# Kernel tuning notes

Measured on AMD Instinct MI355X. Metric: run time of the kernel, lower is better.

The kernel has to match this reference:

```python
import jax, jax.numpy as jnp
import numpy as np

B, S, C = 4, 4096, 1024   # batch, input_size (seq len), channels
H, D, DK = 16, 64, 256    # nhead, head dim, dim_k (Linformer projection)


def setup_inputs() -> dict:
    key = jax.random.key(0)
    ks = jax.random.split(key, 9)
    s_in = 1.0 / np.sqrt(C)
    s_e = 1.0 / np.sqrt(S)
    return {
        'x':   jax.random.normal(ks[0], (B, S, C), jnp.float32),
        # per-head Q/K/V projection weights (Linear(channels, dim, bias=False))
        'Wq':  jax.random.normal(ks[1], (H, D, C), jnp.float32) * s_in,
        'Wk':  jax.random.normal(ks[2], (H, D, C), jnp.float32) * s_in,
        'Wv':  jax.random.normal(ks[3], (H, D, C), jnp.float32) * s_in,
        # shared (layerwise) E/F Linear(input_size, dim_k) with bias
        'E_w': jax.random.normal(ks[4], (DK, S), jnp.float32) * s_e,
        'E_b': jnp.zeros((DK,), jnp.float32),
        'F_w': jax.random.normal(ks[5], (DK, S), jnp.float32) * s_e,
        'F_b': jnp.zeros((DK,), jnp.float32),
        # output projection Linear(dim*nhead, channels)
        'Wo':  jax.random.normal(ks[6], (C, H * D), jnp.float32) * (1.0 / np.sqrt(H * D)),
        'bo':  jnp.zeros((C,), jnp.float32),
    }


def reference(x, Wq, Wk, Wv, E_w, E_b, F_w, F_b, Wo, bo):
    b, s, c = x.shape
    h, d, _ = Wq.shape
    # per-head projections (vectorized over the Python head loop)
    Q = jnp.einsum('bsc,hdc->bhsd', x, Wq)            # [B,H,S,D]
    Kt = jnp.einsum('bsc,hdc->bhds', x, Wk)           # K already transposed: [B,H,D,S]
    Vt = jnp.einsum('bsc,hdc->bhds', x, Wv)           # [B,H,D,S]
    # Linformer low-rank projections along the sequence axis
    Kp = jnp.einsum('bhds,ks->bhdk', Kt, E_w) + E_b   # [B,H,D,DK]
    Vp = jnp.einsum('bhds,ks->bhdk', Vt, F_w) + F_b   # [B,H,D,DK]
    scores = jnp.einsum('bhsd,bhdk->bhsk', Q, Kp) / jnp.sqrt(jnp.asarray(d, x.dtype))
    P = jax.nn.softmax(scores, axis=-1)               # softmax over projected dim_k
    head_out = jnp.einsum('bhsk,bhdk->bhsd', P, Vp)   # [B,H,S,D]
    out = head_out.transpose(0, 2, 1, 3).reshape(b, s, h * d)  # concat heads
    return out @ Wo.T + bo
```

## Files before the change

### kernel.cpp

```cpp
#include <hip/hip_runtime.h>
#include <stdint.h>

typedef __attribute__((ext_vector_type(8))) short bf16x8;
typedef __attribute__((ext_vector_type(4))) float f32x4;
typedef __attribute__((ext_vector_type(16))) float f32x16;

__device__ __forceinline__ unsigned short f2b(float f) {
  union { float f; uint32_t u; } v; v.f = f;
  uint32_t u = v.u;
  return (unsigned short)((u + 0x7FFFu + ((u >> 16) & 1u)) >> 16);
}

__device__ __forceinline__ void gll16(const unsigned short* gsrc, unsigned short* lds_uniform) {
  __builtin_amdgcn_global_load_lds(
      (const __attribute__((address_space(1))) uint32_t*)gsrc,
      (__attribute__((address_space(3))) uint32_t*)lds_uniform,
      16, 0, 0);
}

#define MFMA(a, b, c) __builtin_amdgcn_mfma_f32_16x16x32_bf16((a), (b), (c), 0, 0, 0)
#define MFMA32(a, b, c) __builtin_amdgcn_mfma_f32_32x32x16_bf16((a), (b), (c), 0, 0, 0)

__global__ void cast_x_dual(const float* __restrict__ x,
                            unsigned short* __restrict__ xb,
                            unsigned short* __restrict__ xT) {
  __shared__ unsigned short tile[64][65];
  const int st = blockIdx.x * 64;
  const int ct = blockIdx.y * 64;
  const int b = blockIdx.z;
  const int t = threadIdx.x;
#pragma unroll
  for (int it = 0; it < 4; ++it) {
    int linear = (it * 256 + t) * 4;
    int r = linear >> 6, c = linear & 63;
    float4 v = *(const float4*)(x + ((size_t)(b * 4096 + st + r)) * 1024 + ct + c);
    ushort4 o;
    o.x = f2b(v.x); o.y = f2b(v.y); o.z = f2b(v.z); o.w = f2b(v.w);
    *(ushort4*)(xb + ((size_t)(b * 4096 + st + r)) * 1024 + ct + c) = o;
    tile[r][c] = o.x; tile[r][c + 1] = o.y; tile[r][c + 2] = o.z; tile[r][c + 3] = o.w;
  }
  __syncthreads();
#pragma unroll
  for (int it = 0; it < 4; ++it) {
    int linear = (it * 256 + t) * 4;
    int r = linear >> 6, c = linear & 63;
    ushort4 o;
    o.x = tile[c][r]; o.y = tile[c + 1][r]; o.z = tile[c + 2][r]; o.w = tile[c + 3][r];
    *(ushort4*)(xT + ((size_t)b * 1024 + ct + r) * 4096 + st + c) = o;
  }
}

__global__ void cast6(const float* __restrict__ s0, const float* __restrict__ s1,
                      const float* __restrict__ s2, const float* __restrict__ s3,
                      const float* __restrict__ s4, const float* __restrict__ s5,
                      const float* __restrict__ E_b, const float* __restrict__ F_b,
                      unsigned short* __restrict__ d0, unsigned short* __restrict__ d1,
                      unsigned short* __restrict__ d2, unsigned short* __restrict__ d3,
                      unsigned short* __restrict__ d4, unsigned short* __restrict__ d5,
                      float* __restrict__ EFbias) {
  if (blockIdx.y == 6) {
    if (blockIdx.x == 0) {
      int t = threadIdx.x;
      EFbias[t] = E_b[t];
      EFbias[256 + t] = F_b[t];
    }
    return;
  }
  const float* src; unsigned short* dst; float sc = 1.0f;
  switch (blockIdx.y) {
    case 0: src = s0; dst = d0; sc = 0.18033688011112042f; break;
    case 1: src = s1; dst = d1; break;
    case 2: src = s2; dst = d2; break;
    case 3: src = s3; dst = d3; break;
    case 4: src = s4; dst = d4; break;
    default: src = s5; dst = d5; break;
  }
  int i = (blockIdx.x * 256 + threadIdx.x) * 4;
  float4 v = *(const float4*)(src + i);
  ushort4 o;
  o.x = f2b(v.x * sc); o.y = f2b(v.y * sc); o.z = f2b(v.z * sc); o.w = f2b(v.w * sc);
  *(ushort4*)(dst + i) = o;
}

template <int BIAS, bool OBF16>
__global__ __launch_bounds__(256, 2) void gemm_bt(
    const unsigned short* __restrict__ A, const unsigned short* __restrict__ B,
    void* __restrict__ Cout, const float* __restrict__ bias,
    int M, int N, int K, int lda, int ldb, int ldc,
    long long sA, long long sB, long long sC) {
  __shared__ unsigned short Asm_[2][128 * 32];
  __shared__ unsigned short Bsm_[2][128 * 32];
  const int tid = threadIdx.x;
  const int wave = tid >> 6, lane = tid & 63;
  const int g = lane >> 4, l15 = lane & 15;
  const int bm = blockIdx.x * 128, bn = blockIdx.y * 128;
  const unsigned short* Ab = A + (size_t)blockIdx.z * sA;
  const unsigned short* Bb = B + (size_t)blockIdx.z * sB;
  const int wm = (wave >> 1) * 64, wn = (wave & 1) * 64;

  const int rr0 = wave * 16 + (lane >> 2);
  const int rr1 = rr0 + 64;
  const int sl0 = (lane & 3) ^ ((rr0 >> 1) & 3);
  const int sl1 = (lane & 3) ^ ((rr1 >> 1) & 3);

#define BT_STAGE(T, BUF)                                                          \
  {                                                                               \
    int kt_ = (T) * 32;                                                           \
    gll16(Ab + (size_t)(bm + rr0) * lda + kt_ + sl0 * 8, Asm_[BUF] + wave * 512); \
    gll16(Bb + (size_t)(bn + rr0) * ldb + kt_ + sl0 * 8, Bsm_[BUF] + wave * 512); \
    gll16(Ab + (size_t)(bm + rr1) * lda + kt_ + sl1 * 8, Asm_[BUF] + (wave + 4) * 512); \
    gll16(Bb + (size_t)(bn + rr1) * ldb + kt_ + sl1 * 8, Bsm_[BUF] + (wave + 4) * 512); \
  }

  f32x4 acc[4][4];
#pragma unroll
  for (int i = 0; i < 4; ++i)
#pragma unroll
    for (int j = 0; j < 4; ++j) acc[i][j] = (f32x4){0.f, 0.f, 0.f, 0.f};

  const int nt = K >> 5;
  BT_STAGE(0, 0);
  for (int t = 0; t < nt; ++t) {
    const int cur = t & 1;
    if (t + 1 < nt) {
      BT_STAGE(t + 1, cur ^ 1);
      asm volatile("s_waitcnt vmcnt(4)" ::: "memory");
    } else {
      asm volatile("s_waitcnt vmcnt(0)" ::: "memory");
    }
    __builtin_amdgcn_s_barrier();
    asm volatile("" ::: "memory");

    bf16x8 af[4], bfr[4];
    const char* Ac = (const char*)Asm_[cur];
    const char* Bc = (const char*)Bsm_[cur];
#pragma unroll
    for (int mi = 0; mi < 4; ++mi) {
      int m = wm + mi * 16 + l15;
      af[mi] = *(const bf16x8*)(Ac + m * 64 + ((g ^ ((m >> 1) & 3)) << 4));
    }
#pragma unroll
    for (int ni = 0; ni < 4; ++ni) {
      int n = wn + ni * 16 + l15;
      bfr[ni] = *(const bf16x8*)(Bc + n * 64 + ((g ^ ((n >> 1) & 3)) << 4));
    }
#pragma unroll
    for (int mi = 0; mi < 4; ++mi)
#pragma unroll
      for (int ni = 0; ni < 4; ++ni)
        acc[mi][ni] = MFMA(af[mi], bfr[ni], acc[mi][ni]);

    asm volatile("" ::: "memory");
    __builtin_amdgcn_s_barrier();
  }
#undef BT_STAGE

  if (OBF16) {
    unsigned short* C = (unsigned short*)Cout + (size_t)blockIdx.z * sC;
#pragma unroll
    for (int mi = 0; mi < 4; ++mi)
#pragma unroll
      for (int r = 0; r < 4; ++r) {
        int row = bm + wm + mi * 16 + g * 4 + r;
        float rb = (BIAS == 1) ? bias[row] : 0.f;
#pragma unroll
        for (int ni = 0; ni < 4; ++ni) {
          int col = bn + wn + ni * 16 + l15;
          float v = acc[mi][ni][r] + rb + ((BIAS == 2) ? bias[col] : 0.f);
          C[(size_t)row * ldc + col] = f2b(v);
        }
      }
  } else {
    float* C = (float*)Cout + (size_t)blockIdx.z * sC;
#pragma unroll
    for (int mi = 0; mi < 4; ++mi)
#pragma unroll
      for (int r = 0; r < 4; ++r) {
        int row = bm + wm + mi * 16 + g * 4 + r;
        float rb = (BIAS == 1) ? bias[row] : 0.f;
#pragma unroll
        for (int ni = 0; ni < 4; ++ni) {
          int col = bn + wn + ni * 16 + l15;
          C[(size_t)row * ldc + col] = acc[mi][ni][r] + rb + ((BIAS == 2) ? bias[col] : 0.f);
        }
      }
  }
}

__global__ __launch_bounds__(256, 2) void gemm_xef_splitk(
    const unsigned short* __restrict__ A,
    const unsigned short* __restrict__ B,
    float* __restrict__ Cpart) {
  __shared__ unsigned short Asm_[2][128 * 32];
  __shared__ unsigned short Bsm_[2][128 * 32];
  const int tid = threadIdx.x;
  const int wave = tid >> 6, lane = tid & 63;
  const int g = lane >> 4, l15 = lane & 15;
  const int bm = blockIdx.x * 128, bn = blockIdx.y * 128;
  const int z = blockIdx.z, split = z >> 2, b = z & 3;
  const unsigned short* Ab = A + split * 1024;
  const unsigned short* Bb = B + (size_t)b * 1024 * 4096 + split * 1024;
  const int wm = (wave >> 1) * 64, wn = (wave & 1) * 64;

  const int rr0 = wave * 16 + (lane >> 2);
  const int rr1 = rr0 + 64;
  const int sl0 = (lane & 3) ^ ((rr0 >> 1) & 3);
  const int sl1 = (lane & 3) ^ ((rr1 >> 1) & 3);

#define XEF_STAGE(T, BUF)                                                           \
  {                                                                                 \
    int kt_ = (T) * 32;                                                             \
    gll16(Ab + (size_t)(bm + rr0) * 4096 + kt_ + sl0 * 8, Asm_[BUF] + wave * 512);  \
    gll16(Bb + (size_t)(bn + rr0) * 4096 + kt_ + sl0 * 8, Bsm_[BUF] + wave * 512);  \
    gll16(Ab + (size_t)(bm + rr1) * 4096 + kt_ + sl1 * 8, Asm_[BUF] + (wave + 4) * 512); \
    gll16(Bb + (size_t)(bn + rr1) * 4096 + kt_ + sl1 * 8, Bsm_[BUF] + (wave + 4) * 512); \
  }

  f32x4 acc[4][4];
#pragma unroll
  for (int i = 0; i < 4; ++i)
#pragma unroll
    for (int j = 0; j < 4; ++j) acc[i][j] = (f32x4){0.f, 0.f, 0.f, 0.f};

  const int nt = 32;
  XEF_STAGE(0, 0);
  for (int t = 0; t < nt; ++t) {
    const int cur = t & 1;
    if (t + 1 < nt) {
      XEF_STAGE(t + 1, cur ^ 1);
      asm volatile("s_waitcnt vmcnt(4)" ::: "memory");
    } else {
      asm volatile("s_waitcnt vmcnt(0)" ::: "memory");
    }
    __builtin_amdgcn_s_barrier();
    asm volatile("" ::: "memory");

    bf16x8 af[4], bfr[4];
    const char* Ac = (const char*)Asm_[cur];
    const char* Bc = (const char*)Bsm_[cur];
#pragma unroll
    for (int mi = 0; mi < 4; ++mi) {
      int m = wm + mi * 16 + l15;
      af[mi] = *(const bf16x8*)(Ac + m * 64 + ((g ^ ((m >> 1) & 3)) << 4));
    }
#pragma unroll
    for (int ni = 0; ni < 4; ++ni) {
      int n = wn + ni * 16 + l15;
      bfr[ni] = *(const bf16x8*)(Bc + n * 64 + ((g ^ ((n >> 1) & 3)) << 4));
    }
#pragma unroll
    for (int mi = 0; mi < 4; ++mi)
#pragma unroll
      for (int ni = 0; ni < 4; ++ni)
        acc[mi][ni] = MFMA(af[mi], bfr[ni], acc[mi][ni]);

    asm volatile("" ::: "memory");
    __builtin_amdgcn_s_barrier();
  }
#undef XEF_STAGE

  float* C = Cpart + (size_t)z * (512 * 1024);
#pragma unroll
  for (int mi = 0; mi < 4; ++mi)
#pragma unroll
    for (int r = 0; r < 4; ++r) {
      int row = bm + wm + mi * 16 + g * 4 + r;
#pragma unroll
      for (int ni = 0; ni < 4; ++ni) {
        int col = bn + wn + ni * 16 + l15;
        C[(size_t)row * 1024 + col] = acc[mi][ni][r];
      }
    }
}

__global__ void reduce_xef(const float* __restrict__ P,
                           const float* __restrict__ bias,
                           unsigned short* __restrict__ out) {
  int t = blockIdx.x * 256 + threadIdx.x;
  size_t flat = (size_t)t * 4;
  float4 s = *(const float4*)(P + flat);
#pragma unroll
  for (int sp = 1; sp < 4; ++sp) {
    float4 v = *(const float4*)(P + (size_t)sp * 2097152 + flat);
    s.x += v.x; s.y += v.y; s.z += v.z; s.w += v.w;
  }
  float rb = bias[(flat >> 10) & 511];
  ushort4 o;
  o.x = f2b(s.x + rb); o.y = f2b(s.y + rb);
  o.z = f2b(s.z + rb); o.w = f2b(s.w + rb);
  *(ushort4*)(out + flat) = o;
}

template <int BIAS, bool OBF16, int CMODE>
__global__ __launch_bounds__(256, 4) void gemm_bt64(
    const unsigned short* __restrict__ A, const unsigned short* __restrict__ B,
    void* __restrict__ Cout, const float* __restrict__ bias,
    int M, int N, int K, int lda, int ldb, int ldc,
    long long sA, long long sB, long long sC) {
  __shared__ unsigned short Asm_[2][64 * 32];
  __shared__ unsigned short Bsm_[2][64 * 32];
  const int tid = threadIdx.x;
  const int wave = tid >> 6, lane = tid & 63;
  const int g = lane >> 4, l15 = lane & 15;
  const int bm = blockIdx.x * 64, bn = blockIdx.y * 64;
  const unsigned short* Ab = A + (size_t)blockIdx.z * sA;
  const unsigned short* Bb = B + (size_t)blockIdx.z * sB;
  const int wm = (wave >> 1) * 32, wn = (wave & 1) * 32;

  const int rr = wave * 16 + (lane >> 2);
  const int sl = (lane & 3) ^ ((rr >> 1) & 3);

#define BT64_STAGE(T, BUF)                                                      \
  {                                                                             \
    int kt_ = (T) * 32;                                                         \
    gll16(Ab + (size_t)(bm + rr) * lda + kt_ + sl * 8, Asm_[BUF] + wave * 512); \
    gll16(Bb + (size_t)(bn + rr) * ldb + kt_ + sl * 8, Bsm_[BUF] + wave * 512); \
  }

  f32x4 acc[2][2];
#pragma unroll
  for (int i = 0; i < 2; ++i)
#pragma unroll
    for (int j = 0; j < 2; ++j) acc[i][j] = (f32x4){0.f, 0.f, 0.f, 0.f};

  const int nt = K >> 5;
  BT64_STAGE(0, 0);
  for (int t = 0; t < nt; ++t) {
    const int cur = t & 1;
    if (t + 1 < nt) {
      BT64_STAGE(t + 1, cur ^ 1);
      asm volatile("s_waitcnt vmcnt(2)" ::: "memory");
    } else {
      asm volatile("s_waitcnt vmcnt(0)" ::: "memory");
    }
    __builtin_amdgcn_s_barrier();
    asm volatile("" ::: "memory");

    bf16x8 af[2], bfr[2];
    const char* Ac = (const char*)Asm_[cur];
    const char* Bc = (const char*)Bsm_[cur];
#pragma unroll
    for (int mi = 0; mi < 2; ++mi) {
      int m = wm + mi * 16 + l15;
      af[mi] = *(const bf16x8*)(Ac + m * 64 + ((g ^ ((m >> 1) & 3)) << 4));
    }
#pragma unroll
    for (int ni = 0; ni < 2; ++ni) {
      int n = wn + ni * 16 + l15;
      bfr[ni] = *(const bf16x8*)(Bc + n * 64 + ((g ^ ((n >> 1) & 3)) << 4));
    }
#pragma unroll
    for (int mi = 0; mi < 2; ++mi)
#pragma unroll
      for (int ni = 0; ni < 2; ++ni)
        acc[mi][ni] = MFMA(af[mi], bfr[ni], acc[mi][ni]);

    asm volatile("" ::: "memory");
    __builtin_amdgcn_s_barrier();
  }
#undef BT64_STAGE

#pragma unroll
  for (int mi = 0; mi < 2; ++mi)
#pragma unroll
    for (int r = 0; r < 4; ++r) {
      int row = bm + wm + mi * 16 + g * 4 + r;
      float rb = (BIAS == 1) ? bias[row] : 0.f;
#pragma unroll
      for (int ni = 0; ni < 2; ++ni) {
        int col = bn + wn + ni * 16 + l15;
        float v = acc[mi][ni][r] + rb + ((BIAS == 2) ? bias[col] : 0.f);
        size_t idx;
        if (CMODE == 1) {
          idx = (size_t)(col >> 6) * ((size_t)M * 64) + (size_t)row * 64 + (col & 63);
        } else if (CMODE == 2) {
          int cl = col & 15;
          int cp = (cl & 3) | ((cl & 4) << 1) | ((cl & 8) >> 1);
          idx = (size_t)row * ldc + (col & ~15) + cp;
        } else {
          idx = (size_t)row * ldc + col;
        }
        if (OBF16) ((unsigned short*)Cout + (size_t)blockIdx.z * sC)[idx] = f2b(v);
        else       ((float*)Cout + (size_t)blockIdx.z * sC)[idx] = v;
      }
    }
}

__global__ __launch_bounds__(256, 4) void attn_kernel(
    const unsigned short* __restrict__ q,
    const unsigned short* __restrict__ kp,
    const unsigned short* __restrict__ vp,
    unsigned short* __restrict__ ho) {
  __shared__ unsigned short Ksm[256 * 64];
  __shared__ float Lsm[4 * 32];

  const int tid = threadIdx.x;
  const int wave = tid >> 6, lane = tid & 63;
  const int l31 = lane & 31, hi = lane >> 5;
  const int x = blockIdx.x;
  const int bh = (x & 7) + ((x >> 8) << 3);
  const int qq = (x >> 3) & 31;
  const int b = bh >> 4, h = bh & 15;
  const int s0 = qq * 128;

  const unsigned short* kph = kp + (size_t)bh * (256 * 64);
  const unsigned short* vph = vp + (size_t)bh * (64 * 256);

  {
    const int r = (lane >> 3), sl = (lane & 7) ^ (lane >> 3);
#pragma unroll
    for (int it = 0; it < 8; ++it) {
      int c = it * 4 + wave;
      gll16(kph + (c * 8 + r) * 64 + sl * 8, Ksm + c * 512);
    }
  }

  const int srow = s0 + wave * 32 + l31;
  const unsigned short* qrow = q + (size_t)(b * 4096 + srow) * 1024 + h * 64;
  bf16x8 qf[4];
#pragma unroll
  for (int dc = 0; dc < 4; ++dc)
    qf[dc] = *(const bf16x8*)(qrow + dc * 16 + hi * 8);

  __syncthreads();

  f32x16 ho0 = {0,0,0,0,0,0,0,0,0,0,0,0,0,0,0,0};
  f32x16 ho1 = {0,0,0,0,0,0,0,0,0,0,0,0,0,0,0,0};
  float sum = 0.f;

#pragma unroll
  for (int t = 0; t < 8; ++t) {
    bf16x8 vf00 = *(const bf16x8*)(vph + (size_t)l31 * 256 + (t * 2 + 0) * 16 + hi * 8);
    bf16x8 vf01 = *(const bf16x8*)(vph + (size_t)l31 * 256 + (t * 2 + 1) * 16 + hi * 8);
    bf16x8 vf10 = *(const bf16x8*)(vph + (size_t)(32 + l31) * 256 + (t * 2 + 0) * 16 + hi * 8);
    bf16x8 vf11 = *(const bf16x8*)(vph + (size_t)(32 + l31) * 256 + (t * 2 + 1) * 16 + hi * 8);

    f32x16 qk = {0,0,0,0,0,0,0,0,0,0,0,0,0,0,0,0};
    const int krow = t * 32 + l31;
    const char* kbase = (const char*)Ksm + krow * 128;
#pragma unroll
    for (int dc = 0; dc < 4; ++dc) {
      bf16x8 kf = *(const bf16x8*)(kbase + (((dc * 2 + hi) ^ (l31 & 7)) << 4));
      qk = MFMA32(kf, qf[dc], qk);
    }

    uint32_t pk[8];
#pragma unroll
    for (int j = 0; j < 8; ++j) {
      float e0 = exp2f(qk[2 * j]);
      float e1 = exp2f(qk[2 * j + 1]);
      sum += e0 + e1;
      asm("v_cvt_pk_bf16_f32 %0, %1, %2" : "=v"(pk[j]) : "v"(e0), "v"(e1));
    }
    union { uint32_t u[4]; bf16x8 v; } ua, ub;
    ua.u[0] = pk[0]; ua.u[1] = pk[1]; ua.u[2] = pk[2]; ua.u[3] = pk[3];
    ub.u[0] = pk[4]; ub.u[1] = pk[5]; ub.u[2] = pk[6]; ub.u[3] = pk[7];

    ho0 = MFMA32(ua.v, vf00, ho0);
    ho0 = MFMA32(ub.v, vf01, ho0);
    ho1 = MFMA32(ua.v, vf10, ho1);
    ho1 = MFMA32(ub.v, vf11, ho1);
  }

  sum += __shfl_xor(sum, 32);
  if (lane < 32) Lsm[wave * 32 + lane] = sum;

  float rl[16];
#pragma unroll
  for (int g = 0; g < 4; ++g) {
    float4 d4 = *(const float4*)&Lsm[wave * 32 + g * 8 + hi * 4];
    rl[g * 4 + 0] = __builtin_amdgcn_rcpf(d4.x);
    rl[g * 4 + 1] = __builtin_amdgcn_rcpf(d4.y);
    rl[g * 4 + 2] = __builtin_amdgcn_rcpf(d4.z);
    rl[g * 4 + 3] = __builtin_amdgcn_rcpf(d4.w);
  }

  unsigned short* hob = ho + (size_t)(b * 4096 + s0 + wave * 32) * 1024 + h * 64 + l31;
#pragma unroll
  for (int reg = 0; reg < 16; ++reg) {
    int srw = (reg & 3) + 8 * (reg >> 2) + 4 * hi;
    hob[(size_t)srw * 1024]      = f2b(ho0[reg] * rl[reg]);
    hob[(size_t)srw * 1024 + 32] = f2b(ho1[reg] * rl[reg]);
  }
}

extern "C" void kernel_launch(void* const* d_in, const int* in_sizes, int n_in,
                              void* d_out, int out_size, void* d_ws, size_t ws_size,
                              hipStream_t stream) {
  (void)in_sizes; (void)n_in; (void)out_size; (void)ws_size;
  const float* x   = (const float*)d_in[0];
  const float* Wq  = (const float*)d_in[1];
  const float* Wk  = (const float*)d_in[2];
  const float* Wv  = (const float*)d_in[3];
  const float* E_w = (const float*)d_in[4];
  const float* E_b = (const float*)d_in[5];
  const float* F_w = (const float*)d_in[6];
  const float* F_b = (const float*)d_in[7];
  const float* Wo  = (const float*)d_in[8];
  const float* bo  = (const float*)d_in[9];
  float* out = (float*)d_out;

  char* ws = (char*)d_ws;
  unsigned short* xb   = (unsigned short*)(ws);
  unsigned short* xT   = (unsigned short*)(ws + 33554432);
  unsigned short* Qb   = (unsigned short*)(ws + 67108864);
  unsigned short* Wqb  = (unsigned short*)(ws + 100663296);
  unsigned short* Wkb  = (unsigned short*)(ws + 102760448);
  unsigned short* Wvb  = (unsigned short*)(ws + 104857600);
  unsigned short* Wob  = (unsigned short*)(ws + 106954752);
  unsigned short* EFb  = (unsigned short*)(ws + 109051904);
  unsigned short* xEF  = (unsigned short*)(ws + 113246208);
  unsigned short* Kp   = (unsigned short*)(ws + 117440512);
  unsigned short* Vp   = (unsigned short*)(ws + 119537664);
  float*          EFbias = (float*)(ws + 121634816);
  float*          Ppart  = (float*)(ws + 121700352);
  unsigned short* HO   = xb;

  cast_x_dual<<<dim3(64, 16, 4), 256, 0, stream>>>(x, xb, xT);
  cast6<<<dim3(1024, 7), 256, 0, stream>>>(
      Wq, Wk, Wv, E_w, F_w, Wo, E_b, F_b,
      Wqb, Wkb, Wvb, EFb, EFb + 2097152 / 2, Wob, EFbias);

  gemm_bt<0, true><<<dim3(128, 8, 1), 256, 0, stream>>>(
      xb, Wqb, Qb, nullptr, 16384, 1024, 1024, 1024, 1024, 1024, 0, 0, 0);

  gemm_xef_splitk<<<dim3(4, 8, 16), 256, 0, stream>>>(EFb, xT, Ppart);
  reduce_xef<<<dim3(2048, 1, 1), 256, 0, stream>>>(Ppart, EFbias, xEF);

  gemm_bt64<0, true, 1><<<dim3(4, 16, 4), 256, 0, stream>>>(
      xEF, Wkb, Kp, nullptr, 256, 1024, 1024, 1024, 1024, 1024,
      512LL * 1024, 0LL, 256LL * 1024);

  gemm_bt64<0, true, 2><<<dim3(16, 4, 4), 256, 0, stream>>>(
      Wvb, xEF + 256 * 1024, Vp, nullptr, 1024, 256, 1024, 1024, 1024, 256,
      0LL, 512LL * 1024, 1024LL * 256);

  attn_kernel<<<dim3(2048, 1, 1), 256, 0, stream>>>(Qb, Kp, Vp, HO);

  gemm_bt<2, false><<<dim3(128, 8, 1), 256, 0, stream>>>(
      HO, Wob, out, bo, 16384, 1024, 1024, 1024, 1024, 1024, 0, 0, 0);
}
```

Measured before the change: 229.1 us.

## Use 256x256 tiled 512-thread GEMM for Q and output projections

Replaces the 128x128 four-wave GEMM with a 256x256 tile, eight-wave kernel that processes K in 64-wide steps split into two LDS sub-panels. Next-stage global-to-LDS loads are interleaved into the MFMA loop, and MFMA issue gets raised wave priority. The aim is higher arithmetic intensity and fewer global loads per FLOP for the two large 16384x1024x1024 GEMMs. The trade-off is a smaller grid of 256 blocks, heavy LDS use that allows about one block per CU, and more accumulator registers.

```diff
diff --git a/kernel.cpp b/kernel.cpp
--- a/kernel.cpp
+++ b/kernel.cpp
@@ -83,108 +83,115 @@
 }
 
 template <int BIAS, bool OBF16>
-__global__ __launch_bounds__(256, 2) void gemm_bt(
+__global__ __launch_bounds__(512, 2) void gemm_bt256(
     const unsigned short* __restrict__ A, const unsigned short* __restrict__ B,
     void* __restrict__ Cout, const float* __restrict__ bias,
-    int M, int N, int K, int lda, int ldb, int ldc,
-    long long sA, long long sB, long long sC) {
-  __shared__ unsigned short Asm_[2][128 * 32];
-  __shared__ unsigned short Bsm_[2][128 * 32];
+    int K, int lda, int ldb, int ldc) {
+  __shared__ unsigned short Asm_[2][2][256 * 32];
+  __shared__ unsigned short Bsm_[2][2][256 * 32];
   const int tid = threadIdx.x;
   const int wave = tid >> 6, lane = tid & 63;
-  const int g = lane >> 4, l15 = lane & 15;
-  const int bm = blockIdx.x * 128, bn = blockIdx.y * 128;
-  const unsigned short* Ab = A + (size_t)blockIdx.z * sA;
-  const unsigned short* Bb = B + (size_t)blockIdx.z * sB;
-  const int wm = (wave >> 1) * 64, wn = (wave & 1) * 64;
-
-  const int rr0 = wave * 16 + (lane >> 2);
-  const int rr1 = rr0 + 64;
-  const int sl0 = (lane & 3) ^ ((rr0 >> 1) & 3);
-  const int sl1 = (lane & 3) ^ ((rr1 >> 1) & 3);
-
-#define BT_STAGE(T, BUF)                                                          \
-  {                                                                               \
-    int kt_ = (T) * 32;                                                           \
-    gll16(Ab + (size_t)(bm + rr0) * lda + kt_ + sl0 * 8, Asm_[BUF] + wave * 512); \
-    gll16(Bb + (size_t)(bn + rr0) * ldb + kt_ + sl0 * 8, Bsm_[BUF] + wave * 512); \
-    gll16(Ab + (size_t)(bm + rr1) * lda + kt_ + sl1 * 8, Asm_[BUF] + (wave + 4) * 512); \
-    gll16(Bb + (size_t)(bn + rr1) * ldb + kt_ + sl1 * 8, Bsm_[BUF] + (wave + 4) * 512); \
-  }
-
-  f32x4 acc[4][4];
-#pragma unroll
-  for (int i = 0; i < 4; ++i)
+  const int g = (lane >> 4) & 3, l15 = lane & 15;
+  const int wmi = wave >> 2, wni = wave & 3;
+  const int bm = blockIdx.x * 256, bn = blockIdx.y * 256;
+
+  const int rc = lane >> 2;
+
+#define STG256(XA, H, J, T, BUF)                                              \
+  {                                                                           \
+    int k2_ = wave * 2 + (J);                                                 \
+    int p_ = k2_ >> 3, cc_ = k2_ & 7;                                         \
+    int rr_ = (H) * 128 + cc_ * 16 + rc;                                      \
+    int sl_ = (lane & 3) ^ ((rr_ >> 1) & 3);                                  \
+    const unsigned short* s_ = (XA)                                           \
+        ? A + (size_t)(bm + rr_) * lda + (T) * 64 + p_ * 32 + sl_ * 8         \
+        : B + (size_t)(bn + rr_) * ldb + (T) * 64 + p_ * 32 + sl_ * 8;        \
+    unsigned short* d_ = ((XA) ? &Asm_[BUF][p_][0] : &Bsm_[BUF][p_][0])       \
+                         + ((H) * 128 + cc_ * 16) * 32;                       \
+    gll16(s_, d_);                                                            \
+  }
+
+  f32x4 acc[8][4];
+#pragma unroll
+  for (int i = 0; i < 8; ++i)
 #pragma unroll
     for (int j = 0; j < 4; ++j) acc[i][j] = (f32x4){0.f, 0.f, 0.f, 0.f};
 
-  const int nt = K >> 5;
-  BT_STAGE(0, 0);
+  const int nt = K >> 6;
+  STG256(1, 0, 0, 0, 0) STG256(1, 0, 1, 0, 0)
+  STG256(0, 0, 0, 0, 0) STG256(0, 0, 1, 0, 0)
+  STG256(1, 1, 0, 0, 0) STG256(1, 1, 1, 0, 0)
+  STG256(0, 1, 0, 0, 0) STG256(0, 1, 1, 0, 0)
+  asm volatile("s_waitcnt vmcnt(0)" ::: "memory");
+  __builtin_amdgcn_s_barrier();
+  asm volatile("" ::: "memory");
+
   for (int t = 0; t < nt; ++t) {
-    const int cur = t & 1;
-    if (t + 1 < nt) {
-      BT_STAGE(t + 1, cur ^ 1);
-      asm volatile("s_waitcnt vmcnt(4)" ::: "memory");
-    } else {
-      asm volatile("s_waitcnt vmcnt(0)" ::: "memory");
-    }
+    const int cur = t & 1, nxt = cur ^ 1;
+    const char* Ap0 = (const char*)&Asm_[cur][0][0];
+    const char* Ap1 = (const char*)&Asm_[cur][1][0];
+    const char* Bp0 = (const char*)&Bsm_[cur][0][0];
+    const char* Bp1 = (const char*)&Bsm_[cur][1][0];
+    const bool more = (t + 1 < nt);
+
+    bf16x8 bf[4][2];
+#pragma unroll
+    for (int ni = 0; ni < 4; ++ni) {
+      int n = wni * 64 + ni * 16 + l15;
+      int sw = ((g ^ ((n >> 1) & 3)) << 4);
+      bf[ni][0] = *(const bf16x8*)(Bp0 + n * 64 + sw);
+      bf[ni][1] = *(const bf16x8*)(Bp1 + n * 64 + sw);
+    }
+
+#pragma unroll
+    for (int q = 0; q < 4; ++q) {
+      if (q == 0 && more) {
+        STG256(1, 0, 0, t + 1, nxt) STG256(1, 0, 1, t + 1, nxt)
+        STG256(0, 0, 0, t + 1, nxt) STG256(0, 0, 1, t + 1, nxt)
+      }
+      if (q == 1 && more) {
+        STG256(1, 1, 0, t + 1, nxt) STG256(1, 1, 1, t + 1, nxt)
+        STG256(0, 1, 0, t + 1, nxt) STG256(0, 1, 1, t + 1, nxt)
+      }
+      bf16x8 af[2][2];
+#pragma unroll
+      for (int mi2 = 0; mi2 < 2; ++mi2) {
+        int m = wmi * 128 + (q * 2 + mi2) * 16 + l15;
+        int sw = ((g ^ ((m >> 1) & 3)) << 4);
+        af[mi2][0] = *(const bf16x8*)(Ap0 + m * 64 + sw);
+        af[mi2][1] = *(const bf16x8*)(Ap1 + m * 64 + sw);
+      }
+      __builtin_amdgcn_s_setprio(1);
+#pragma unroll
+      for (int mi2 = 0; mi2 < 2; ++mi2)
+#pragma unroll
+        for (int ni = 0; ni < 4; ++ni) {
+          acc[q * 2 + mi2][ni] = MFMA(af[mi2][0], bf[ni][0], acc[q * 2 + mi2][ni]);
+          acc[q * 2 + mi2][ni] = MFMA(af[mi2][1], bf[ni][1], acc[q * 2 + mi2][ni]);
+        }
+      __builtin_amdgcn_s_setprio(0);
+    }
+
+    asm volatile("s_waitcnt vmcnt(0)" ::: "memory");
     __builtin_amdgcn_s_barrier();
     asm volatile("" ::: "memory");
-
-    bf16x8 af[4], bfr[4];
-    const char* Ac = (const char*)Asm_[cur];
-    const char* Bc = (const char*)Bsm_[cur];
-#pragma unroll
-    for (int mi = 0; mi < 4; ++mi) {
-      int m = wm + mi * 16 + l15;
-      af[mi] = *(const bf16x8*)(Ac + m * 64 + ((g ^ ((m >> 1) & 3)) << 4));
-    }
-#pragma unroll
-    for (int ni = 0; ni < 4; ++ni) {
-      int n = wn + ni * 16 + l15;
-      bfr[ni] = *(const bf16x8*)(Bc + n * 64 + ((g ^ ((n >> 1) & 3)) << 4));
-    }
-#pragma unroll
-    for (int mi = 0; mi < 4; ++mi)
-#pragma unroll
-      for (int ni = 0; ni < 4; ++ni)
-        acc[mi][ni] = MFMA(af[mi], bfr[ni], acc[mi][ni]);
-
-    asm volatile("" ::: "memory");
-    __builtin_amdgcn_s_barrier();
-  }
-#undef BT_STAGE
-
-  if (OBF16) {
-    unsigned short* C = (unsigned short*)Cout + (size_t)blockIdx.z * sC;
-#pragma unroll
-    for (int mi = 0; mi < 4; ++mi)
-#pragma unroll
-      for (int r = 0; r < 4; ++r) {
-        int row = bm + wm + mi * 16 + g * 4 + r;
-        float rb = (BIAS == 1) ? bias[row] : 0.f;
-#pragma unroll
-        for (int ni = 0; ni < 4; ++ni) {
-          int col = bn + wn + ni * 16 + l15;
-          float v = acc[mi][ni][r] + rb + ((BIAS == 2) ? bias[col] : 0.f);
-          C[(size_t)row * ldc + col] = f2b(v);
-        }
+  }
+#undef STG256
+
+#pragma unroll
+  for (int mf = 0; mf < 8; ++mf)
+#pragma unroll
+    for (int r = 0; r < 4; ++r) {
+      int row = bm + wmi * 128 + mf * 16 + g * 4 + r;
+      float rb = (BIAS == 1) ? bias[row] : 0.f;
+#pragma unroll
+      for (int ni = 0; ni < 4; ++ni) {
+        int col = bn + wni * 64 + ni * 16 + l15;
+        float v = acc[mf][ni][r] + rb + ((BIAS == 2) ? bias[col] : 0.f);
+        if (OBF16) ((unsigned short*)Cout)[(size_t)row * ldc + col] = f2b(v);
+        else       ((float*)Cout)[(size_t)row * ldc + col] = v;
       }
-  } else {
-    float* C = (float*)Cout + (size_t)blockIdx.z * sC;
-#pragma unroll
-    for (int mi = 0; mi < 4; ++mi)
-#pragma unroll
-      for (int r = 0; r < 4; ++r) {
-        int row = bm + wm + mi * 16 + g * 4 + r;
-        float rb = (BIAS == 1) ? bias[row] : 0.f;
-#pragma unroll
-        for (int ni = 0; ni < 4; ++ni) {
-          int col = bn + wn + ni * 16 + l15;
-          C[(size_t)row * ldc + col] = acc[mi][ni][r] + rb + ((BIAS == 2) ? bias[col] : 0.f);
-        }
-      }
-  }
+    }
 }
 
 __global__ __launch_bounds__(256, 2) void gemm_xef_splitk(
@@ -521,8 +528,8 @@
       Wq, Wk, Wv, E_w, F_w, Wo, E_b, F_b,
       Wqb, Wkb, Wvb, EFb, EFb + 2097152 / 2, Wob, EFbias);
 
-  gemm_bt<0, true><<<dim3(128, 8, 1), 256, 0, stream>>>(
-      xb, Wqb, Qb, nullptr, 16384, 1024, 1024, 1024, 1024, 1024, 0, 0, 0);
+  gemm_bt256<0, true><<<dim3(64, 4), 512, 0, stream>>>(
+      xb, Wqb, Qb, nullptr, 1024, 1024, 1024, 1024);
 
   gemm_xef_splitk<<<dim3(4, 8, 16), 256, 0, stream>>>(EFb, xT, Ppart);
   reduce_xef<<<dim3(2048, 1, 1), 256, 0, stream>>>(Ppart, EFbias, xEF);
@@ -537,6 +544,6 @@
 
   attn_kernel<<<dim3(2048, 1, 1), 256, 0, stream>>>(Qb, Kp, Vp, HO);
 
-  gemm_bt<2, false><<<dim3(128, 8, 1), 256, 0, stream>>>(
-      HO, Wob, out, bo, 16384, 1024, 1024, 1024, 1024, 1024, 0, 0, 0);
-}
+  gemm_bt256<2, false><<<dim3(64, 4), 512, 0, stream>>>(
+      HO, Wob, out, bo, 1024, 1024, 1024, 1024);
+}
```

Measured after the change: 224.0 us. -2.2%, faster.
